# Kernel tuning notes

Measured on AMD Instinct MI355X. Metric: run time of the kernel, lower is better.

Reference implementation:

```python
import jax, jax.numpy as jnp
import numpy as np
import math


def _lsq(x, s, bit, all_positive):
    # LSQ fake-quant: scale -> clamp -> round (STE) -> dequant
    if all_positive:
        qn, qp = 0.0, float(2 ** bit - 1)
    else:
        qn, qp = -float(2 ** (bit - 1)), float(2 ** (bit - 1) - 1)
    g = 1.0 / math.sqrt(x.size * qp)  # grad-scale factor (static)
    sg = s * g
    s_eff = sg + jax.lax.stop_gradient(s - sg)  # fwd = s, grad scaled by g
    xq = jnp.clip(x / s_eff, qn, qp)
    xq = xq + jax.lax.stop_gradient(jnp.round(xq) - xq)  # round with STE
    return xq * s_eff


def _conv(x, w, stride):
    return jax.lax.conv_general_dilated(
        x, w, window_strides=(stride, stride), padding='VALID',
        dimension_numbers=('NCHW', 'OIHW', 'NCHW'))


def setup_inputs() -> dict:
    key = jax.random.key(0)
    ks = jax.random.split(key, 5)
    B = 65536
    x = jax.random.normal(ks[0], (B, 1, 28, 28), dtype=jnp.float32)
    w1 = jax.random.normal(ks[1], (4, 1, 5, 5), dtype=jnp.float32) * 0.2
    w2 = jax.random.normal(ks[2], (8, 4, 3, 3), dtype=jnp.float32) * 0.2
    fc_w = jax.random.normal(ks[3], (10, 200), dtype=jnp.float32) * 0.07
    fc_b = jax.random.normal(ks[4], (10,), dtype=jnp.float32) * 0.01
    one = jnp.ones((1,), dtype=jnp.float32)
    return {"x": x, "w1": w1, "w2": w2, "fc_w": fc_w, "fc_b": fc_b,
            "s_in": one * 0.05, "s_w1": one * 0.02, "s_a1": one * 0.05,
            "s_w2": one * 0.02, "s_a2": one * 0.05, "s_fc": one * 0.02}


def reference(x, w1, w2, fc_w, fc_b, s_in, s_w1, s_a1, s_w2, s_a2, s_fc):
    x = _lsq(x, s_in, 8, False)
    x = _conv(x, _lsq(w1, s_w1, 8, False), 2)          # [B,4,12,12]
    x = jax.nn.relu(_lsq(x, s_a1, 8, True))
    x = _conv(x, _lsq(w2, s_w2, 8, False), 2)          # [B,8,5,5]
    x = jax.nn.relu(_lsq(x, s_a2, 8, True))
    x = x.reshape(x.shape[0], -1)                      # [B,200]
    return x @ _lsq(fc_w, s_fc, 8, False).T + fc_b     # [B,10]
```

## Files before the change

kernel.cpp:

```cpp
#include <hip/hip_runtime.h>
#include <math.h>

#define G  8
#define NG 8

#if __has_builtin(__builtin_amdgcn_sdot4)
__device__ __forceinline__ int dot4(unsigned a, unsigned b, int c) {
    return __builtin_amdgcn_sdot4((int)a, (int)b, c, false);
}
#else
__device__ __forceinline__ int dot4(unsigned a, unsigned b, int c) {
    c += (int)(signed char)(a & 255u)         * (int)(signed char)(b & 255u);
    c += (int)(signed char)((a >> 8) & 255u)  * (int)(signed char)((b >> 8) & 255u);
    c += (int)(signed char)((a >> 16) & 255u) * (int)(signed char)((b >> 16) & 255u);
    c += (int)(signed char)(a >> 24)          * (int)(signed char)(b >> 24);
    return c;
}
#endif

__device__ __forceinline__ void wave_fence() {
    asm volatile("s_waitcnt lgkmcnt(0)" ::: "memory");
}

__device__ __forceinline__ float seff(float s, float gf) {
    float sg = s * gf;
    return sg + (s - sg);
}
__device__ __forceinline__ unsigned q8(float v, float s, float rs) {
    float q0 = v * rs;
    float r  = fmaf(-s, q0, v);
    float y  = fmaf(r, rs, q0);
    y = fminf(fmaxf(y, -128.f), 127.f);
    float t = y + 12582912.0f;
    return __float_as_uint(t);
}
__device__ __forceinline__ unsigned pack4(unsigned a, unsigned b, unsigned c, unsigned d) {
    return (a & 255u) | ((b & 255u) << 8) | ((c & 255u) << 16) | (d << 24);
}
__device__ __forceinline__ int mround(int acc, double r) {
    double t = fma((double)acc, r, 6755399441055744.0);
    return (int)__double_as_longlong(t);
}

extern "C" __global__ __launch_bounds__(256, 4)
void qcnn_fused(const float* __restrict__ x,  const float* __restrict__ w1,
                const float* __restrict__ w2, const float* __restrict__ fcw,
                const float* __restrict__ fcb,
                const float* __restrict__ s_in, const float* __restrict__ s_w1,
                const float* __restrict__ s_a1, const float* __restrict__ s_w2,
                const float* __restrict__ s_a2, const float* __restrict__ s_fc,
                float* __restrict__ out, int B,
                float gx, float gw1, float ga1, float gw2, float ga2, float gfc)
{
    __shared__ unsigned xs[2][G*196];
    __shared__ unsigned a1p[G*144];
    __shared__ unsigned a2p[G*50];
    __shared__ __align__(16) unsigned w1pk[4][5][4];
    __shared__ unsigned w2p[8][9];
    __shared__ unsigned fcp[10][50];
    __shared__ int K2s[8];
    __shared__ int K3s[10];
    __shared__ float fcbs[10];

    const int tid = threadIdx.x;
    const int g   = tid >> 5;
    const int t   = tid & 31;

    const float sx  = seff(s_in[0], gx);
    const float sw1 = seff(s_w1[0], gw1);
    const float sa1 = seff(s_a1[0], ga1);
    const float sw2 = seff(s_w2[0], gw2);
    const float sa2 = seff(s_a2[0], ga2);
    const float sfc = seff(s_fc[0], gfc);
    const float rsx = 1.0f / sx;
    const float rw1 = 1.0f / sw1;
    const float rw2 = 1.0f / sw2;
    const float rfc = 1.0f / sfc;
    const double r1 = (double)sx  * (double)sw1 / (double)sa1;
    const double r2 = (double)sa1 * (double)sw2 / (double)sa2;
    const double r3 = (double)sa2 * (double)sfc;

    const long long gbase = (long long)blockIdx.x * NG;

    float4 Rv0, Rv1, Rv2, Rv3, Rv4, Rv5, Rv6;
    auto stage_load = [&](long long grp) {
        const long long img = grp * G + g;
        if (img >= B) return;
        const float4* xp = (const float4*)x + img * 196;
        Rv0 = xp[t];        Rv1 = xp[t + 32];  Rv2 = xp[t + 64];
        Rv3 = xp[t + 96];   Rv4 = xp[t + 128]; Rv5 = xp[t + 160];
        if (t < 4) Rv6 = xp[t + 192];
    };
    auto stage_write = [&](long long grp, int buf) {
        const long long img = grp * G + g;
        if (img >= B) return;
        unsigned* dst = &xs[buf][g*196];
        float4 v;
        v = Rv0; dst[t]       = pack4(q8(v.x,sx,rsx), q8(v.y,sx,rsx), q8(v.z,sx,rsx), q8(v.w,sx,rsx));
        v = Rv1; dst[t + 32]  = pack4(q8(v.x,sx,rsx), q8(v.y,sx,rsx), q8(v.z,sx,rsx), q8(v.w,sx,rsx));
        v = Rv2; dst[t + 64]  = pack4(q8(v.x,sx,rsx), q8(v.y,sx,rsx), q8(v.z,sx,rsx), q8(v.w,sx,rsx));
        v = Rv3; dst[t + 96]  = pack4(q8(v.x,sx,rsx), q8(v.y,sx,rsx), q8(v.z,sx,rsx), q8(v.w,sx,rsx));
        v = Rv4; dst[t + 128] = pack4(q8(v.x,sx,rsx), q8(v.y,sx,rsx), q8(v.z,sx,rsx), q8(v.w,sx,rsx));
        v = Rv5; dst[t + 160] = pack4(q8(v.x,sx,rsx), q8(v.y,sx,rsx), q8(v.z,sx,rsx), q8(v.w,sx,rsx));
        if (t < 4) {
            v = Rv6;
            dst[t + 192] = pack4(q8(v.x,sx,rsx), q8(v.y,sx,rsx), q8(v.z,sx,rsx), q8(v.w,sx,rsx));
        }
    };

    stage_load(gbase);

    if (tid < 80) {
        const int c = tid / 20, rem = tid % 20, ky = rem >> 2, vv = rem & 3;
        const float* wr = w1 + c*25 + ky*5;
        unsigned b[5];
        #pragma unroll
        for (int k = 0; k < 5; ++k) b[k] = q8(wr[k], sw1, rw1) & 255u;
        unsigned pk;
        if      (vv == 0) pk = b[0] | (b[1] << 8) | (b[2] << 16) | (b[3] << 24);
        else if (vv == 1) pk = b[4];
        else if (vv == 2) pk = (b[0] << 16) | (b[1] << 24);
        else              pk = b[2] | (b[3] << 8) | (b[4] << 16);
        w1pk[c][ky][vv] = pk;
    } else if (tid < 152) {
        const int d = tid - 80, oc = d / 9, tap = d % 9;
        unsigned pk = 0;
        #pragma unroll
        for (int ic = 0; ic < 4; ++ic)
            pk |= (q8(w2[oc*36 + ic*9 + tap], sw2, rw2) & 255u) << (8*ic);
        w2p[oc][tap] = pk;
    }
    if (tid < 10) fcbs[tid] = fcb[tid];
    for (int i = tid; i < 500; i += 256) {
        const int o = i / 50, kd = i % 50;
        const float* fr = fcw + o*200 + kd*4;
        fcp[o][kd] = pack4(q8(fr[0],sfc,rfc), q8(fr[1],sfc,rfc),
                           q8(fr[2],sfc,rfc), q8(fr[3],sfc,rfc));
    }
    __syncthreads();
    if (tid < 8) {
        int s = 0;
        #pragma unroll
        for (int d = 0; d < 9; ++d) s = dot4(w2p[tid][d], 0x01010101u, s);
        K2s[tid] = s << 7;
    } else if (tid < 18) {
        const int o = tid - 8;
        int s = 0;
        for (int d = 0; d < 50; ++d) s = dot4(fcp[o][d], 0x01010101u, s);
        K3s[o] = s << 7;
    }
    __syncthreads();
    stage_write(gbase, 0);
    wave_fence();

    int cur = 0;
    for (int it = 0; it < NG; ++it) {
        const long long grp = gbase + it;
        if (grp * G >= B) break;
        const bool act = (grp * G + g) < B;

        if (it + 1 < NG) stage_load(grp + 1);

        if (act) {
            const int c  = t & 3;
            const int h  = (t >> 2) & 1;
            const int y0 = t >> 3;
            uint4 W[5];
            #pragma unroll
            for (int ky = 0; ky < 5; ++ky)
                W[ky] = *(const uint4*)&w1pk[c][ky][0];
            const unsigned* xb = &xs[cur][g*196];
            #pragma unroll
            for (int k = 0; k < 3; ++k) {
                const int y = y0 + 4*k;
                int acc[6] = {0,0,0,0,0,0};
                #pragma unroll
                for (int ky = 0; ky < 5; ++ky) {
                    const unsigned* rp = xb + (2*y + ky)*7 + 3*h;
                    const unsigned L0 = rp[0], L1 = rp[1], L2 = rp[2], L3 = rp[3];
                    acc[0] = dot4(L1, W[ky].y, dot4(L0, W[ky].x, acc[0]));
                    acc[1] = dot4(L1, W[ky].w, dot4(L0, W[ky].z, acc[1]));
                    acc[2] = dot4(L2, W[ky].y, dot4(L1, W[ky].x, acc[2]));
                    acc[3] = dot4(L2, W[ky].w, dot4(L1, W[ky].z, acc[3]));
                    acc[4] = dot4(L3, W[ky].y, dot4(L2, W[ky].x, acc[4]));
                    acc[5] = dot4(L3, W[ky].w, dot4(L2, W[ky].z, acc[5]));
                }
                unsigned char* dst = (unsigned char*)a1p + (g*144 + y*12 + 6*h)*4 + c;
                #pragma unroll
                for (int m = 0; m < 6; ++m) {
                    int q = mround(acc[m], r1);
                    q = min(max(q, 0), 255);
                    dst[4*m] = (unsigned char)(q - 128);
                }
            }
        }
        wave_fence();

        if (act) {
            const int oc = t >> 2;
            unsigned wv[9];
            #pragma unroll
            for (int d = 0; d < 9; ++d) wv[d] = w2p[oc][d];
            const int k2 = K2s[oc];
            const unsigned* base = &a1p[g*144];
            unsigned char* dstb = (unsigned char*)a2p + g*200 + oc*25;
            #pragma unroll
            for (int pass = 0; pass < 2; ++pass) {
                const int y = pass ? 4 : (t & 3);
                if (pass && (t & 3) != 0) break;
                unsigned rw[3][12];
                #pragma unroll
                for (int ky = 0; ky < 3; ++ky) {
                    const uint4* rp = (const uint4*)&base[(2*y + ky)*12];
                    uint4 A = rp[0], Bv = rp[1], Cv = rp[2];
                    rw[ky][0]=A.x;  rw[ky][1]=A.y;  rw[ky][2]=A.z;  rw[ky][3]=A.w;
                    rw[ky][4]=Bv.x; rw[ky][5]=Bv.y; rw[ky][6]=Bv.z; rw[ky][7]=Bv.w;
                    rw[ky][8]=Cv.x; rw[ky][9]=Cv.y; rw[ky][10]=Cv.z; rw[ky][11]=Cv.w;
                }
                #pragma unroll
                for (int jx = 0; jx < 5; ++jx) {
                    int acc = k2;
                    #pragma unroll
                    for (int ky = 0; ky < 3; ++ky)
                        #pragma unroll
                        for (int kx = 0; kx < 3; ++kx)
                            acc = dot4(rw[ky][2*jx + kx], wv[ky*3 + kx], acc);
                    int q = mround(acc, r2);
                    q = min(max(q, 0), 255);
                    dstb[y*5 + jx] = (unsigned char)(q - 128);
                }
            }
        }
        wave_fence();

        if (act && t < 30) {
            const int part = t / 10;
            const int o    = t - part*10;
            const int k0   = part * 17;
            const int nk   = (part == 2) ? 16 : 17;
            int acc = 0;
            for (int ki = 0; ki < nk; ++ki) {
                const int k = k0 + ki;
                acc = dot4(a2p[g*50 + k], fcp[o][k], acc);
            }
            const int self0 = (g & 1) * 32 + o;
            const int s1 = __shfl(acc, self0 + 10);
            const int s2 = __shfl(acc, self0 + 20);
            if (part == 0) {
                const int total = acc + s1 + s2 + K3s[o];
                const double oo = (double)total * r3 + (double)fcbs[o];
                out[(grp*G + g)*10 + o] = (float)oo;
            }
        }

        if (it + 1 < NG) {
            stage_write(grp + 1, cur ^ 1);
            wave_fence();
        }
        cur ^= 1;
    }
}

extern "C" void kernel_launch(void* const* d_in, const int* in_sizes, int n_in,
                              void* d_out, int out_size, void* d_ws, size_t ws_size,
                              hipStream_t stream) {
    const float* x    = (const float*)d_in[0];
    const float* w1   = (const float*)d_in[1];
    const float* w2   = (const float*)d_in[2];
    const float* fcw  = (const float*)d_in[3];
    const float* fcb  = (const float*)d_in[4];
    const float* s_in = (const float*)d_in[5];
    const float* s_w1 = (const float*)d_in[6];
    const float* s_a1 = (const float*)d_in[7];
    const float* s_w2 = (const float*)d_in[8];
    const float* s_a2 = (const float*)d_in[9];
    const float* s_fc = (const float*)d_in[10];

    const int B = in_sizes[0] / 784;
    const float gx  = (float)(1.0 / sqrt((double)B * 784.0 * 127.0));
    const float gw1 = (float)(1.0 / sqrt(100.0 * 127.0));
    const float ga1 = (float)(1.0 / sqrt((double)B * 576.0 * 255.0));
    const float gw2 = (float)(1.0 / sqrt(288.0 * 127.0));
    const float ga2 = (float)(1.0 / sqrt((double)B * 200.0 * 255.0));
    const float gfc = (float)(1.0 / sqrt(2000.0 * 127.0));

    const int imgs_per_block = G * NG;
    const int grid = (B + imgs_per_block - 1) / imgs_per_block;
    qcnn_fused<<<grid, 256, 0, stream>>>(x, w1, w2, fcw, fcb,
                                         s_in, s_w1, s_a1, s_w2, s_a2, s_fc,
                                         (float*)d_out, B,
                                         gx, gw1, ga1, gw2, ga2, gfc);
}
```

Measured before the change: 55.61 us.

## Pad input rows in LDS for 128-bit conv1 loads and vectorize FC dot

Re-lays out each quantized input image in shared memory as 28 rows of 8 words, duplicating column 3 so each conv1 thread reads its 4-word window with one aligned uint4 load instead of four scalar loads. Pads a2p and fcp rows to 52 words so the FC partial sums can use uint4 loads over 16 words each, plus a 2-word tail. Conv1 and conv2 weights are hoisted into registers once, outside the group loop. The cost is more LDS per block (which may reduce occupancy), extra work per store when writing the input, and more register pressure.

```diff
diff --git a/kernel.cpp b/kernel.cpp
--- a/kernel.cpp
+++ b/kernel.cpp
@@ -52,12 +52,12 @@
                 float* __restrict__ out, int B,
                 float gx, float gw1, float ga1, float gw2, float ga2, float gfc)
 {
-    __shared__ unsigned xs[2][G*196];
+    __shared__ unsigned xs[2][G*224];
     __shared__ unsigned a1p[G*144];
-    __shared__ unsigned a2p[G*50];
+    __shared__ unsigned a2p[G*52];
     __shared__ __align__(16) unsigned w1pk[4][5][4];
     __shared__ unsigned w2p[8][9];
-    __shared__ unsigned fcp[10][50];
+    __shared__ unsigned fcp[10][52];
     __shared__ int K2s[8];
     __shared__ int K3s[10];
     __shared__ float fcbs[10];
@@ -94,17 +94,23 @@
     auto stage_write = [&](long long grp, int buf) {
         const long long img = grp * G + g;
         if (img >= B) return;
-        unsigned* dst = &xs[buf][g*196];
+        unsigned* dst0 = &xs[buf][g*224];
+        auto put = [&](int i, unsigned pk) {
+            const int row = i / 7, col = i % 7;
+            unsigned* dr = dst0 + row*8;
+            dr[col + (col > 3 ? 1 : 0)] = pk;
+            if (col == 3) dr[4] = pk;
+        };
         float4 v;
-        v = Rv0; dst[t]       = pack4(q8(v.x,sx,rsx), q8(v.y,sx,rsx), q8(v.z,sx,rsx), q8(v.w,sx,rsx));
-        v = Rv1; dst[t + 32]  = pack4(q8(v.x,sx,rsx), q8(v.y,sx,rsx), q8(v.z,sx,rsx), q8(v.w,sx,rsx));
-        v = Rv2; dst[t + 64]  = pack4(q8(v.x,sx,rsx), q8(v.y,sx,rsx), q8(v.z,sx,rsx), q8(v.w,sx,rsx));
-        v = Rv3; dst[t + 96]  = pack4(q8(v.x,sx,rsx), q8(v.y,sx,rsx), q8(v.z,sx,rsx), q8(v.w,sx,rsx));
-        v = Rv4; dst[t + 128] = pack4(q8(v.x,sx,rsx), q8(v.y,sx,rsx), q8(v.z,sx,rsx), q8(v.w,sx,rsx));
-        v = Rv5; dst[t + 160] = pack4(q8(v.x,sx,rsx), q8(v.y,sx,rsx), q8(v.z,sx,rsx), q8(v.w,sx,rsx));
+        v = Rv0; put(t,       pack4(q8(v.x,sx,rsx), q8(v.y,sx,rsx), q8(v.z,sx,rsx), q8(v.w,sx,rsx)));
+        v = Rv1; put(t + 32,  pack4(q8(v.x,sx,rsx), q8(v.y,sx,rsx), q8(v.z,sx,rsx), q8(v.w,sx,rsx)));
+        v = Rv2; put(t + 64,  pack4(q8(v.x,sx,rsx), q8(v.y,sx,rsx), q8(v.z,sx,rsx), q8(v.w,sx,rsx)));
+        v = Rv3; put(t + 96,  pack4(q8(v.x,sx,rsx), q8(v.y,sx,rsx), q8(v.z,sx,rsx), q8(v.w,sx,rsx)));
+        v = Rv4; put(t + 128, pack4(q8(v.x,sx,rsx), q8(v.y,sx,rsx), q8(v.z,sx,rsx), q8(v.w,sx,rsx)));
+        v = Rv5; put(t + 160, pack4(q8(v.x,sx,rsx), q8(v.y,sx,rsx), q8(v.z,sx,rsx), q8(v.w,sx,rsx)));
         if (t < 4) {
             v = Rv6;
-            dst[t + 192] = pack4(q8(v.x,sx,rsx), q8(v.y,sx,rsx), q8(v.z,sx,rsx), q8(v.w,sx,rsx));
+            put(t + 192, pack4(q8(v.x,sx,rsx), q8(v.y,sx,rsx), q8(v.z,sx,rsx), q8(v.w,sx,rsx)));
         }
     };
 
@@ -150,6 +156,20 @@
         K3s[o] = s << 7;
     }
     __syncthreads();
+
+    const int c1  = t & 3;
+    const int h1  = (t >> 2) & 1;
+    const int y01 = t >> 3;
+    uint4 W1r[5];
+    #pragma unroll
+    for (int ky = 0; ky < 5; ++ky)
+        W1r[ky] = *(const uint4*)&w1pk[c1][ky][0];
+    const int oc2 = t >> 2;
+    unsigned wv2[9];
+    #pragma unroll
+    for (int d = 0; d < 9; ++d) wv2[d] = w2p[oc2][d];
+    const int k22 = K2s[oc2];
+
     stage_write(gbase, 0);
     wave_fence();
 
@@ -162,30 +182,23 @@
         if (it + 1 < NG) stage_load(grp + 1);
 
         if (act) {
-            const int c  = t & 3;
-            const int h  = (t >> 2) & 1;
-            const int y0 = t >> 3;
-            uint4 W[5];
-            #pragma unroll
-            for (int ky = 0; ky < 5; ++ky)
-                W[ky] = *(const uint4*)&w1pk[c][ky][0];
-            const unsigned* xb = &xs[cur][g*196];
+            const unsigned* xb = &xs[cur][g*224];
             #pragma unroll
             for (int k = 0; k < 3; ++k) {
-                const int y = y0 + 4*k;
+                const int y = y01 + 4*k;
                 int acc[6] = {0,0,0,0,0,0};
                 #pragma unroll
                 for (int ky = 0; ky < 5; ++ky) {
-                    const unsigned* rp = xb + (2*y + ky)*7 + 3*h;
-                    const unsigned L0 = rp[0], L1 = rp[1], L2 = rp[2], L3 = rp[3];
-                    acc[0] = dot4(L1, W[ky].y, dot4(L0, W[ky].x, acc[0]));
-                    acc[1] = dot4(L1, W[ky].w, dot4(L0, W[ky].z, acc[1]));
-                    acc[2] = dot4(L2, W[ky].y, dot4(L1, W[ky].x, acc[2]));
-                    acc[3] = dot4(L2, W[ky].w, dot4(L1, W[ky].z, acc[3]));
-                    acc[4] = dot4(L3, W[ky].y, dot4(L2, W[ky].x, acc[4]));
-                    acc[5] = dot4(L3, W[ky].w, dot4(L2, W[ky].z, acc[5]));
+                    const uint4 R = *(const uint4*)&xb[(2*y + ky)*8 + 4*h1];
+                    const uint4 W = W1r[ky];
+                    acc[0] = dot4(R.y, W.y, dot4(R.x, W.x, acc[0]));
+                    acc[1] = dot4(R.y, W.w, dot4(R.x, W.z, acc[1]));
+                    acc[2] = dot4(R.z, W.y, dot4(R.y, W.x, acc[2]));
+                    acc[3] = dot4(R.z, W.w, dot4(R.y, W.z, acc[3]));
+                    acc[4] = dot4(R.w, W.y, dot4(R.z, W.x, acc[4]));
+                    acc[5] = dot4(R.w, W.w, dot4(R.z, W.z, acc[5]));
                 }
-                unsigned char* dst = (unsigned char*)a1p + (g*144 + y*12 + 6*h)*4 + c;
+                unsigned char* dst = (unsigned char*)a1p + (g*144 + y*12 + 6*h1)*4 + c1;
                 #pragma unroll
                 for (int m = 0; m < 6; ++m) {
                     int q = mround(acc[m], r1);
@@ -197,13 +210,8 @@
         wave_fence();
 
         if (act) {
-            const int oc = t >> 2;
-            unsigned wv[9];
-            #pragma unroll
-            for (int d = 0; d < 9; ++d) wv[d] = w2p[oc][d];
-            const int k2 = K2s[oc];
             const unsigned* base = &a1p[g*144];
-            unsigned char* dstb = (unsigned char*)a2p + g*200 + oc*25;
+            unsigned char* dstb = (unsigned char*)a2p + g*208 + oc2*25;
             #pragma unroll
             for (int pass = 0; pass < 2; ++pass) {
                 const int y = pass ? 4 : (t & 3);
@@ -219,12 +227,12 @@
                 }
                 #pragma unroll
                 for (int jx = 0; jx < 5; ++jx) {
-                    int acc = k2;
+                    int acc = k22;
                     #pragma unroll
                     for (int ky = 0; ky < 3; ++ky)
                         #pragma unroll
                         for (int kx = 0; kx < 3; ++kx)
-                            acc = dot4(rw[ky][2*jx + kx], wv[ky*3 + kx], acc);
+                            acc = dot4(rw[ky][2*jx + kx], wv2[ky*3 + kx], acc);
                     int q = mround(acc, r2);
                     q = min(max(q, 0), 255);
                     dstb[y*5 + jx] = (unsigned char)(q - 128);
@@ -236,12 +244,19 @@
         if (act && t < 30) {
             const int part = t / 10;
             const int o    = t - part*10;
-            const int k0   = part * 17;
-            const int nk   = (part == 2) ? 16 : 17;
+            const int k0   = part * 16;
             int acc = 0;
-            for (int ki = 0; ki < nk; ++ki) {
-                const int k = k0 + ki;
-                acc = dot4(a2p[g*50 + k], fcp[o][k], acc);
+            const uint4* ap = (const uint4*)&a2p[g*52 + k0];
+            const uint4* wp = (const uint4*)&fcp[o][k0];
+            #pragma unroll
+            for (int q4 = 0; q4 < 4; ++q4) {
+                uint4 a = ap[q4], w = wp[q4];
+                acc = dot4(a.x, w.x, acc); acc = dot4(a.y, w.y, acc);
+                acc = dot4(a.z, w.z, acc); acc = dot4(a.w, w.w, acc);
+            }
+            if (part == 2) {
+                acc = dot4(a2p[g*52 + 48], fcp[o][48], acc);
+                acc = dot4(a2p[g*52 + 49], fcp[o][49], acc);
             }
             const int self0 = (g & 1) * 32 + o;
             const int s1 = __shfl(acc, self0 + 10);
```

After: 100.2 us. 80.1% more time.
